# Optimization experiments

Hardware: AMD Instinct MI355X
Metric: run time of the kernel (lower is better)

The kernel has to match this reference:

```python
import jax, jax.numpy as jnp
import numpy as np
from jax import lax

D = 300          # embedding dim (data.x.shape[1])
H = 1024         # hidden_state_dim
H2 = H // 2
V_SENSES = 25000   # last_idx_senses
V_GLOBALS = 50000  # last_idx_globals - last_idx_senses
NUM_NODES = 80000
T = 1024           # seq_len (batch=1)


def _lin_init(k, out_f, in_f):
    # torch.nn.Linear default: U(-1/sqrt(in), 1/sqrt(in)) for W and b
    kw, kb = jax.random.split(k)
    lim = 1.0 / np.sqrt(in_f)
    W = jax.random.uniform(kw, (out_f, in_f), jnp.float32, -lim, lim)
    b = jax.random.uniform(kb, (out_f,), jnp.float32, -lim, lim)
    return W, b


def setup_inputs() -> dict:
    key = jax.random.key(0)
    ks = jax.random.split(key, 6)
    X = jax.random.normal(ks[0], (NUM_NODES, D), jnp.float32) * 0.1
    W1, b1 = _lin_init(ks[1], H, D + H)
    W2, b2 = _lin_init(ks[2], H2, H + H2)
    Wg, bg = _lin_init(ks[3], V_GLOBALS, H2)
    Ws, bs = _lin_init(ks[4], V_SENSES, H2)
    indices = jax.random.randint(ks[5], (1, T), 0, NUM_NODES, jnp.int32)
    return {"X": X, "W1": W1, "b1": b1, "W2": W2, "b2": b2,
            "Wg": Wg, "bg": bg, "Ws": Ws, "bs": bs, "indices": indices}


def reference(X, W1, b1, W2, b2, Wg, bg, Ws, bs, indices):
    # Sequential RNN over flattened (batch, seq) steps; memory_h1/h2 start at
    # zeros and carry across all steps (as the in-place .data.copy_ does).
    # Dropout is treated as identity (eval mode).
    idx = indices.reshape(-1)  # [T]

    def step(carry, i):
        h1, h2 = carry  # [H], [H2]
        e = X[i]  # gather current-word embedding, [D]
        h1n = jax.nn.leaky_relu(
            jnp.dot(W1, jnp.concatenate([e, h1])) + b1, negative_slope=0.01)
        h2n = jax.nn.leaky_relu(
            jnp.dot(W2, jnp.concatenate([h1n, h2])) + b2, negative_slope=0.01)
        return (h1n, h2n), h2n

    init = (jnp.zeros((H,), X.dtype), jnp.zeros((H2,), X.dtype))
    _, h2s = lax.scan(step, init, idx)  # h2s: [T, H2]

    # Output projections batched over all timesteps (same math as per-step).
    logp_globals = jax.nn.log_softmax(h2s @ Wg.T + bg, axis=-1)  # [T, V_GLOBALS]
    logp_senses = jax.nn.log_softmax(h2s @ Ws.T + bs, axis=-1)   # [T, V_SENSES]
    return logp_globals, logp_senses
```

## Files before the change

### kernel.cpp

```cpp
#include <hip/hip_runtime.h>
#include <hip/hip_bf16.h>
#include <stdint.h>

#define T_STEPS 1024
#define NH1 1024
#define NH2 512
#define D_IN 300
#define W1_LD 1324
#define W2_LD 1536
#define NVG 50000
#define NVS 25000

typedef unsigned long long u64;
typedef __bf16 bf16x8 __attribute__((ext_vector_type(8)));
typedef short s16x8 __attribute__((ext_vector_type(8)));
typedef float f32x4 __attribute__((ext_vector_type(4)));

__global__ __launch_bounds__(256) void e_kernel(
    const float* __restrict__ X,
    const float* __restrict__ W1,
    const float* __restrict__ b1,
    const int* __restrict__ idx,
    float* __restrict__ E,
    unsigned* __restrict__ ctl)
{
  if (blockIdx.x == 0 && threadIdx.x < 16) ctl[threadIdx.x] = 0u;

  __shared__ float Xs[32 * 300];
  const int rb = blockIdx.x & 7;
  const int tb = blockIdx.x >> 3;
  const int r0 = rb * 128;
  const int t0 = tb * 32;

  for (int t = 0; t < 32; ++t) {
    int node = idx[t0 + t];
    for (int c = threadIdx.x; c < 300; c += 256)
      Xs[t * 300 + c] = X[(size_t)node * D_IN + c];
  }
  __syncthreads();

  const int rl = threadIdx.x & 127;
  const int th = threadIdx.x >> 7;
  const int tbase = th * 16;
  const int r = r0 + rl;

  float acc[16];
  const float bias = b1[r];
#pragma unroll
  for (int tt = 0; tt < 16; ++tt) acc[tt] = bias;

  const float* wrow = W1 + (size_t)r * W1_LD;
  for (int c0 = 0; c0 < 300; c0 += 4) {
    float w0 = wrow[c0 + 0];
    float w1 = wrow[c0 + 1];
    float w2 = wrow[c0 + 2];
    float w3 = wrow[c0 + 3];
#pragma unroll
    for (int tt = 0; tt < 16; ++tt) {
      const float* xr = Xs + (tbase + tt) * 300 + c0;
      acc[tt] += w0 * xr[0] + w1 * xr[1] + w2 * xr[2] + w3 * xr[3];
    }
  }
#pragma unroll
  for (int tt = 0; tt < 16; ++tt)
    E[(size_t)(t0 + tbase + tt) * NH1 + r] = acc[tt];
}

__global__ __launch_bounds__(512, 2) void rnn_kernel(
    const float* __restrict__ W1,
    const float* __restrict__ W2,
    const float* __restrict__ b2,
    const float* __restrict__ E,
    u64* __restrict__ buf1,
    u64* __restrict__ buf2,
    __hip_bfloat16* __restrict__ h2s,
    unsigned* __restrict__ ctl)
{
  __shared__ float lds1[2][NH1];
  __shared__ float lds2[2][NH2];
  __shared__ int s_role;

  if (threadIdx.x == 0) {
    int xcd;
    asm volatile("s_getreg_b32 %0, hwreg(HW_REG_XCC_ID)" : "=s"(xcd));
    xcd &= 7;
    unsigned rk = atomicAdd(&ctl[xcd], 1u);
    int role = -1;
    if (rk < 32u) {
      if (rk == 31u) atomicCAS(&ctl[8], 0u, (unsigned)(xcd + 1));
      unsigned wnr;
      while ((wnr = __hip_atomic_load(&ctl[8], __ATOMIC_RELAXED,
                                      __HIP_MEMORY_SCOPE_AGENT)) == 0u)
        __builtin_amdgcn_s_sleep(16);
      if (wnr == (unsigned)(xcd + 1)) role = (int)rk;
    }
    s_role = role;
  }
  __syncthreads();
  if (s_role < 0) return;
  const int b = s_role;

  const int lane = threadIdx.x & 63;
  const int w = threadIdx.x >> 6;
  const int wvid = b * 8 + w;
  const int r1 = wvid * 4;
  const int r2 = wvid * 2;
  const int oct = (w + b) & 7;

  float w1r[4][16];
#pragma unroll
  for (int i = 0; i < 4; ++i)
#pragma unroll
    for (int j = 0; j < 16; ++j)
      w1r[i][j] = W1[(size_t)(r1 + i) * W1_LD + D_IN + lane + 64 * j];

  float w2r[2][24];
#pragma unroll
  for (int i = 0; i < 2; ++i)
#pragma unroll
    for (int j = 0; j < 24; ++j)
      w2r[i][j] = W2[(size_t)(r2 + i) * W2_LD + lane + 64 * j];

  const float b2a = b2[r2];
  const float b2b = b2[r2 + 1];

  for (int s = 0; s <= T_STEPS; ++s) {
    float ev = 0.f;
    if (s < T_STEPS) ev = E[(size_t)s * NH1 + r1 + (lane & 3)];

    float v1[2] = {0.f, 0.f};
    float v2 = 0.f;
    unsigned miss = 0;
    if (s >= 1) miss |= 0x3u;
    if (s >= 2) miss |= 0x4u;
    const u64* p1 = buf1 + (size_t)(s & 3) * NH1 + 128 * oct + lane;
    const u64* p2 = buf2 + (size_t)((s - 1) & 3) * NH2 + 64 * oct + lane;
    const unsigned tag1 = (unsigned)s;
    const unsigned tag2 = (unsigned)(s - 1);

    while (miss) {
      u64 t1[2], t2;
      asm volatile(
          "global_load_dwordx2 %0, %3, off sc0 sc1\n\t"
          "global_load_dwordx2 %1, %3, off offset:512 sc0 sc1\n\t"
          "global_load_dwordx2 %2, %4, off sc0 sc1\n\t"
          "s_waitcnt vmcnt(0)"
          : "=&v"(t1[0]), "=&v"(t1[1]), "=&v"(t2)
          : "v"(p1), "v"(p2)
          : "memory");
#pragma unroll
      for (int j = 0; j < 2; ++j)
        if ((miss & (1u << j)) && (unsigned)(t1[j] >> 32) == tag1) {
          v1[j] = __uint_as_float((unsigned)t1[j]);
          miss &= ~(1u << j);
        }
      if ((miss & 0x4u) && (unsigned)(t2 >> 32) == tag2) {
        v2 = __uint_as_float((unsigned)t2);
        miss &= ~0x4u;
      }
    }

    const int pb = s & 1;
#pragma unroll
    for (int j = 0; j < 2; ++j) lds1[pb][128 * oct + 64 * j + lane] = v1[j];
    lds2[pb][64 * oct + lane] = v2;
    __syncthreads();

    float a0 = 0.f, a1 = 0.f, a2 = 0.f, a3 = 0.f, a4 = 0.f, a5 = 0.f;
#pragma unroll
    for (int j = 0; j < 16; ++j) {
      float h = lds1[pb][lane + 64 * j];
      a0 += w1r[0][j] * h;
      a1 += w1r[1][j] * h;
      a2 += w1r[2][j] * h;
      a3 += w1r[3][j] * h;
      a4 += w2r[0][j] * h;
      a5 += w2r[1][j] * h;
    }
#pragma unroll
    for (int j = 0; j < 8; ++j) {
      float h = lds2[pb][lane + 64 * j];
      a4 += w2r[0][16 + j] * h;
      a5 += w2r[1][16 + j] * h;
    }

#pragma unroll
    for (int off = 32; off; off >>= 1) {
      a0 += __shfl_xor(a0, off);
      a1 += __shfl_xor(a1, off);
      a2 += __shfl_xor(a2, off);
      a3 += __shfl_xor(a3, off);
    }
    if (s < T_STEPS && lane < 4) {
      float x = (lane == 0 ? a0 : lane == 1 ? a1 : lane == 2 ? a2 : a3) + ev;
      float h = x > 0.f ? x : 0.01f * x;
      u64 pk = ((u64)(unsigned)(s + 1) << 32) | (u64)__float_as_uint(h);
      u64* dst = buf1 + (size_t)((s + 1) & 3) * NH1 + r1 + lane;
      asm volatile("global_store_dwordx2 %0, %1, off sc0"
                   :: "v"(dst), "v"(pk) : "memory");
    }

    if (s >= 1) {
#pragma unroll
      for (int off = 32; off; off >>= 1) {
        a4 += __shfl_xor(a4, off);
        a5 += __shfl_xor(a5, off);
      }
      if (lane >= 4 && lane < 6) {
        int i = lane - 4;
        float x = (i == 0 ? a4 : a5) + (i == 0 ? b2a : b2b);
        float h = x > 0.f ? x : 0.01f * x;
        u64 pk = ((u64)(unsigned)s << 32) | (u64)__float_as_uint(h);
        u64* dst = buf2 + (size_t)(s & 3) * NH2 + r2 + i;
        asm volatile("global_store_dwordx2 %0, %1, off sc0"
                     :: "v"(dst), "v"(pk) : "memory");
        h2s[(size_t)(s - 1) * NH2 + r2 + i] = __float2bfloat16(h);
      }
    }
  }
}

__global__ __launch_bounds__(256, 1) void gemm_kernel(
    const __hip_bfloat16* __restrict__ A,
    const float* __restrict__ B,
    const float* __restrict__ bias,
    float* __restrict__ C,
    int N)
{
  __shared__ short As[256 * 64];
  __shared__ short Bs[128 * 64];
  const int tid = threadIdx.x;
  const int lane = tid & 63;
  const int wv = tid >> 6;
  const int wm = (wv & 1) * 128;
  const int wn = (wv >> 1) * 64;
  const int m0 = blockIdx.x * 256;
  const int n0 = blockIdx.y * 128;
  const int ml = lane & 15;
  const int kq = lane >> 4;

  f32x4 acc[8][4];
#pragma unroll
  for (int i = 0; i < 8; ++i)
#pragma unroll
    for (int j = 0; j < 4; ++j)
      acc[i][j] = (f32x4){0.f, 0.f, 0.f, 0.f};

  for (int kb = 0; kb < 512; kb += 64) {
    __syncthreads();
#pragma unroll
    for (int q = 0; q < 8; ++q) {
      int ch = q * 256 + tid;
      int row = ch >> 3;
      int kc = ch & 7;
      int phys = kc ^ (row & 7);
      s16x8 av = *(const s16x8*)((const short*)A + (size_t)(m0 + row) * 512 + kb + kc * 8);
      *(s16x8*)(As + row * 64 + phys * 8) = av;
    }
#pragma unroll
    for (int q = 0; q < 4; ++q) {
      int ch = q * 256 + tid;
      int row = ch >> 3;
      int kc = ch & 7;
      int phys = kc ^ (row & 7);
      int gr = n0 + row;
      if (gr >= N) gr = N - 1;
      const float* src = B + (size_t)gr * 512 + kb + kc * 8;
      f32x4 f0 = *(const f32x4*)(src);
      f32x4 f1 = *(const f32x4*)(src + 4);
      bf16x8 bv;
      bv[0] = (__bf16)f0[0]; bv[1] = (__bf16)f0[1];
      bv[2] = (__bf16)f0[2]; bv[3] = (__bf16)f0[3];
      bv[4] = (__bf16)f1[0]; bv[5] = (__bf16)f1[1];
      bv[6] = (__bf16)f1[2]; bv[7] = (__bf16)f1[3];
      *(bf16x8*)(Bs + row * 64 + phys * 8) = bv;
    }
    __syncthreads();
#pragma unroll
    for (int ks = 0; ks < 2; ++ks) {
      bf16x8 af[8], bfr[4];
#pragma unroll
      for (int i = 0; i < 8; ++i) {
        int row = wm + 16 * i + ml;
        int phys = (ks * 4 + kq) ^ (row & 7);
        af[i] = *(const bf16x8*)(As + row * 64 + phys * 8);
      }
#pragma unroll
      for (int j = 0; j < 4; ++j) {
        int row = wn + 16 * j + ml;
        int phys = (ks * 4 + kq) ^ (row & 7);
        bfr[j] = *(const bf16x8*)(Bs + row * 64 + phys * 8);
      }
#pragma unroll
      for (int i = 0; i < 8; ++i)
#pragma unroll
        for (int j = 0; j < 4; ++j)
          acc[i][j] = __builtin_amdgcn_mfma_f32_16x16x32_bf16(af[i], bfr[j], acc[i][j], 0, 0, 0);
    }
  }

  float bv[4];
#pragma unroll
  for (int j = 0; j < 4; ++j) {
    int n = n0 + wn + 16 * j + ml;
    bv[j] = (n < N) ? bias[n] : 0.f;
  }
#pragma unroll
  for (int i = 0; i < 8; ++i) {
    int mrow = m0 + wm + 16 * i + kq * 4;
#pragma unroll
    for (int j = 0; j < 4; ++j) {
      int n = n0 + wn + 16 * j + ml;
      if (n < N) {
#pragma unroll
        for (int r = 0; r < 4; ++r)
          C[(size_t)(mrow + r) * N + n] = acc[i][j][r] + bv[j];
      }
    }
  }
}

__global__ __launch_bounds__(256) void norm_kernel(float* __restrict__ out)
{
  const int b = blockIdx.x;
  const int t = b & 1023;
  const int seg = b >> 10;
  const size_t base = seg == 0 ? (size_t)t * NVG
                               : (size_t)1024 * NVG + (size_t)t * NVS;
  const int len = seg == 0 ? NVG : NVS;
  float* p = out + base;
  const int lane = threadIdx.x & 63;
  const int wv = threadIdx.x >> 6;
  __shared__ float red[4];

  float m = -3.0e38f;
  for (int i = threadIdx.x; i < len; i += 256)
    m = fmaxf(m, p[i]);
#pragma unroll
  for (int off = 32; off; off >>= 1) m = fmaxf(m, __shfl_xor(m, off));
  if (lane == 0) red[wv] = m;
  __syncthreads();
  m = fmaxf(fmaxf(red[0], red[1]), fmaxf(red[2], red[3]));
  __syncthreads();

  float sum = 0.f;
  for (int i = threadIdx.x; i < len; i += 256)
    sum += expf(p[i] - m);
#pragma unroll
  for (int off = 32; off; off >>= 1) sum += __shfl_xor(sum, off);
  if (lane == 0) red[wv] = sum;
  __syncthreads();
  sum = red[0] + red[1] + red[2] + red[3];
  const float lse = m + logf(sum);

  for (int i = threadIdx.x; i < len; i += 256)
    p[i] = p[i] - lse;
}

extern "C" void kernel_launch(void* const* d_in, const int* in_sizes, int n_in,
                              void* d_out, int out_size, void* d_ws, size_t ws_size,
                              hipStream_t stream) {
  const float* X  = (const float*)d_in[0];
  const float* W1 = (const float*)d_in[1];
  const float* b1 = (const float*)d_in[2];
  const float* W2 = (const float*)d_in[3];
  const float* b2 = (const float*)d_in[4];
  const float* Wg = (const float*)d_in[5];
  const float* bg = (const float*)d_in[6];
  const float* Ws = (const float*)d_in[7];
  const float* bs = (const float*)d_in[8];
  const int* idx = (const int*)d_in[9];
  float* out = (float*)d_out;

  char* ws = (char*)d_ws;
  float* E = (float*)ws;
  __hip_bfloat16* h2s = (__hip_bfloat16*)(ws + (size_t)4194304);
  u64* buf1 = (u64*)(ws + (size_t)5242880);
  u64* buf2 = (u64*)(ws + (size_t)5275648);
  unsigned* ctl = (unsigned*)(out + (size_t)1024 * (NVG + NVS) - 16);

  e_kernel<<<256, 256, 0, stream>>>(X, W1, b1, idx, E, ctl);
  rnn_kernel<<<256, 512, 0, stream>>>(W1, W2, b2, E, buf1, buf2, h2s, ctl);
  gemm_kernel<<<dim3(4, 391), 256, 0, stream>>>(h2s, Wg, bg, out, NVG);
  gemm_kernel<<<dim3(4, 196), 256, 0, stream>>>(h2s, Ws, bs,
                                                out + (size_t)1024 * NVG, NVS);
  norm_kernel<<<2048, 256, 0, stream>>>(out);
}
```

Baseline: 2.966 ms.

## Pipeline RNN flag polling, pre-convert output weights to bf16, online-softmax norm

```diff
diff --git a/kernel.cpp b/kernel.cpp
--- a/kernel.cpp
+++ b/kernel.cpp
@@ -65,6 +65,29 @@
   for (int tt = 0; tt < 16; ++tt)
     E[(size_t)(t0 + tbase + tt) * NH1 + r] = acc[tt];
 }
+
+#define PISSUE(T)                                                            \
+  asm volatile(                                                              \
+      "global_load_dwordx2 %0, %3, off sc0 sc1\n\t"                          \
+      "global_load_dwordx2 %1, %3, off offset:512 sc0 sc1\n\t"               \
+      "global_load_dwordx2 %2, %4, off sc0 sc1"                              \
+      : "=&v"(T[0]), "=&v"(T[1]), "=&v"(T[2])                                \
+      : "v"(p1), "v"(p2)                                                     \
+      : "memory")
+#define PWAIT3                                                               \
+  do {                                                                       \
+    asm volatile("s_waitcnt vmcnt(3)" ::: "memory");                         \
+    __builtin_amdgcn_sched_barrier(0);                                       \
+  } while (0)
+#define PCHECK(T)                                                            \
+  do {                                                                       \
+    if ((miss & 0x1u) && (unsigned)(T[0] >> 32) == tag1) {                   \
+      v1[0] = __uint_as_float((unsigned)T[0]); miss &= ~0x1u; }              \
+    if ((miss & 0x2u) && (unsigned)(T[1] >> 32) == tag1) {                   \
+      v1[1] = __uint_as_float((unsigned)T[1]); miss &= ~0x2u; }              \
+    if ((miss & 0x4u) && (unsigned)(T[2] >> 32) == tag2) {                   \
+      v2 = __uint_as_float((unsigned)T[2]); miss &= ~0x4u; }                 \
+  } while (0)
 
 __global__ __launch_bounds__(512, 2) void rnn_kernel(
     const float* __restrict__ W1,
@@ -138,26 +161,20 @@
     const unsigned tag1 = (unsigned)s;
     const unsigned tag2 = (unsigned)(s - 1);
 
-    while (miss) {
-      u64 t1[2], t2;
-      asm volatile(
-          "global_load_dwordx2 %0, %3, off sc0 sc1\n\t"
-          "global_load_dwordx2 %1, %3, off offset:512 sc0 sc1\n\t"
-          "global_load_dwordx2 %2, %4, off sc0 sc1\n\t"
-          "s_waitcnt vmcnt(0)"
-          : "=&v"(t1[0]), "=&v"(t1[1]), "=&v"(t2)
-          : "v"(p1), "v"(p2)
-          : "memory");
-#pragma unroll
-      for (int j = 0; j < 2; ++j)
-        if ((miss & (1u << j)) && (unsigned)(t1[j] >> 32) == tag1) {
-          v1[j] = __uint_as_float((unsigned)t1[j]);
-          miss &= ~(1u << j);
-        }
-      if ((miss & 0x4u) && (unsigned)(t2 >> 32) == tag2) {
-        v2 = __uint_as_float((unsigned)t2);
-        miss &= ~0x4u;
-      }
+    if (miss) {
+      u64 tA[3], tB[3];
+      PISSUE(tA);
+      for (;;) {
+        PISSUE(tB);
+        PWAIT3;
+        PCHECK(tA);
+        if (!miss) break;
+        PISSUE(tA);
+        PWAIT3;
+        PCHECK(tB);
+        if (!miss) break;
+      }
+      asm volatile("s_waitcnt vmcnt(0)" ::: "memory");
     }
 
     const int pb = s & 1;
@@ -215,6 +232,115 @@
         asm volatile("global_store_dwordx2 %0, %1, off sc0"
                      :: "v"(dst), "v"(pk) : "memory");
         h2s[(size_t)(s - 1) * NH2 + r2 + i] = __float2bfloat16(h);
+      }
+    }
+  }
+}
+
+__global__ __launch_bounds__(256) void bconv_kernel(
+    const float* __restrict__ B, __hip_bfloat16* __restrict__ Bb, int n8)
+{
+  int stride = gridDim.x * 256;
+  for (int i = blockIdx.x * 256 + threadIdx.x; i < n8; i += stride) {
+    const f32x4* s = (const f32x4*)B + (size_t)i * 2;
+    f32x4 f0 = s[0], f1 = s[1];
+    bf16x8 bv;
+    bv[0] = (__bf16)f0[0]; bv[1] = (__bf16)f0[1];
+    bv[2] = (__bf16)f0[2]; bv[3] = (__bf16)f0[3];
+    bv[4] = (__bf16)f1[0]; bv[5] = (__bf16)f1[1];
+    bv[6] = (__bf16)f1[2]; bv[7] = (__bf16)f1[3];
+    *(bf16x8*)((short*)Bb + (size_t)i * 8) = bv;
+  }
+}
+
+__global__ __launch_bounds__(256, 1) void gemm_bf16_kernel(
+    const __hip_bfloat16* __restrict__ A,
+    const __hip_bfloat16* __restrict__ Bb,
+    const float* __restrict__ bias,
+    float* __restrict__ C,
+    int N)
+{
+  __shared__ short As[256 * 64];
+  __shared__ short Bs[128 * 64];
+  const int tid = threadIdx.x;
+  const int lane = tid & 63;
+  const int wv = tid >> 6;
+  const int wm = (wv & 1) * 128;
+  const int wn = (wv >> 1) * 64;
+  const int m0 = blockIdx.x * 256;
+  const int n0 = blockIdx.y * 128;
+  const int ml = lane & 15;
+  const int kq = lane >> 4;
+
+  f32x4 acc[8][4];
+#pragma unroll
+  for (int i = 0; i < 8; ++i)
+#pragma unroll
+    for (int j = 0; j < 4; ++j)
+      acc[i][j] = (f32x4){0.f, 0.f, 0.f, 0.f};
+
+  for (int kb = 0; kb < 512; kb += 64) {
+    __syncthreads();
+#pragma unroll
+    for (int q = 0; q < 8; ++q) {
+      int ch = q * 256 + tid;
+      int row = ch >> 3;
+      int kc = ch & 7;
+      int phys = kc ^ (row & 7);
+      s16x8 av = *(const s16x8*)((const short*)A + (size_t)(m0 + row) * 512 + kb + kc * 8);
+      *(s16x8*)(As + row * 64 + phys * 8) = av;
+    }
+#pragma unroll
+    for (int q = 0; q < 4; ++q) {
+      int ch = q * 256 + tid;
+      int row = ch >> 3;
+      int kc = ch & 7;
+      int phys = kc ^ (row & 7);
+      int gr = n0 + row;
+      if (gr >= N) gr = N - 1;
+      s16x8 bvv = *(const s16x8*)((const short*)Bb + (size_t)gr * 512 + kb + kc * 8);
+      *(s16x8*)(Bs + row * 64 + phys * 8) = bvv;
+    }
+    __syncthreads();
+#pragma unroll
+    for (int ks = 0; ks < 2; ++ks) {
+      bf16x8 af[8], bfr[4];
+#pragma unroll
+      for (int i = 0; i < 8; ++i) {
+        int row = wm + 16 * i + ml;
+        int phys = (ks * 4 + kq) ^ (row & 7);
+        af[i] = *(const bf16x8*)(As + row * 64 + phys * 8);
+      }
+#pragma unroll
+      for (int j = 0; j < 4; ++j) {
+        int row = wn + 16 * j + ml;
+        int phys = (ks * 4 + kq) ^ (row & 7);
+        bfr[j] = *(const bf16x8*)(Bs + row * 64 + phys * 8);
+      }
+#pragma unroll
+      for (int i = 0; i < 8; ++i)
+#pragma unroll
+        for (int j = 0; j < 4; ++j)
+          acc[i][j] = __builtin_amdgcn_mfma_f32_16x16x32_bf16(af[i], bfr[j], acc[i][j], 0, 0, 0);
+    }
+  }
+
+  float bv[4];
+#pragma unroll
+  for (int j = 0; j < 4; ++j) {
+    int n = n0 + wn + 16 * j + ml;
+    bv[j] = (n < N) ? bias[n] : 0.f;
+  }
+#pragma unroll
+  for (int i = 0; i < 8; ++i) {
+    int mrow = m0 + wm + 16 * i + kq * 4;
+#pragma unroll
+    for (int j = 0; j < 4; ++j) {
+      int n = n0 + wn + 16 * j + ml;
+      if (n < N) {
+#pragma unroll
+        for (int r = 0; r < 4; ++r)
+          C[(size_t)(mrow + r) * N + n] = acc[i][j][r] + bv[j];
       }
     }
   }
@@ -320,41 +446,51 @@
   }
 }
 
-__global__ __launch_bounds__(256) void norm_kernel(float* __restrict__ out)
+__global__ __launch_bounds__(512) void norm_kernel(float* __restrict__ out)
 {
   const int b = blockIdx.x;
   const int t = b & 1023;
   const int seg = b >> 10;
   const size_t base = seg == 0 ? (size_t)t * NVG
                                : (size_t)1024 * NVG + (size_t)t * NVS;
-  const int len = seg == 0 ? NVG : NVS;
-  float* p = out + base;
+  const int len4 = (seg == 0 ? NVG : NVS) >> 2;
+  f32x4* p = (f32x4*)(out + base);
   const int lane = threadIdx.x & 63;
   const int wv = threadIdx.x >> 6;
-  __shared__ float red[4];
-
-  float m = -3.0e38f;
-  for (int i = threadIdx.x; i < len; i += 256)
-    m = fmaxf(m, p[i]);
-#pragma unroll
-  for (int off = 32; off; off >>= 1) m = fmaxf(m, __shfl_xor(m, off));
-  if (lane == 0) red[wv] = m;
+  __shared__ float redm[8], reds[8];
+
+  float m = -3.0e38f, ssum = 0.f;
+  for (int i = threadIdx.x; i < len4; i += 512) {
+    f32x4 v = p[i];
+    float vm = fmaxf(fmaxf(v[0], v[1]), fmaxf(v[2], v[3]));
+    if (vm > m) { ssum *= expf(m - vm); m = vm; }
+    ssum += expf(v[0] - m) + expf(v[1] - m) + expf(v[2] - m) + expf(v[3] - m);
+  }
+#pragma unroll
+  for (int off = 32; off; off >>= 1) {
+    float mo = __shfl_xor(m, off);
+    float so = __shfl_xor(ssum, off);
+    float mn = fmaxf(m, mo);
+    ssum = ssum * expf(m - mn) + so * expf(mo - mn);
+    m = mn;
+  }
+  if (lane == 0) { redm[wv] = m; reds[wv] = ssum; }
   __syncthreads();
-  m = fmaxf(fmaxf(red[0], red[1]), fmaxf(red[2], red[3]));
-  __syncthreads();
-
-  float sum = 0.f;
-  for (int i = threadIdx.x; i < len; i += 256)
-    sum += expf(p[i] - m);
-#pragma unroll
-  for (int off = 32; off; off >>= 1) sum += __shfl_xor(sum, off);
-  if (lane == 0) red[wv] = sum;
-  __syncthreads();
-  sum = red[0] + red[1] + red[2] + red[3];
-  const float lse = m + logf(sum);
-
-  for (int i = threadIdx.x; i < len; i += 256)
-    p[i] = p[i] - lse;
+  float M = redm[0], S = reds[0];
+#pragma unroll
+  for (int k = 1; k < 8; ++k) {
+    float mo = redm[k], so = reds[k];
+    float mn = fmaxf(M, mo);
+    S = S * expf(M - mn) + so * expf(mo - mn);
+    M = mn;
+  }
+  const float lse = M + logf(S);
+
+  for (int i = threadIdx.x; i < len4; i += 512) {
+    f32x4 v = p[i];
+    v[0] -= lse; v[1] -= lse; v[2] -= lse; v[3] -= lse;
+    p[i] = v;
+  }
 }
 
 extern "C" void kernel_launch(void* const* d_in, const int* in_sizes, int n_in,
@@ -377,12 +513,23 @@
   __hip_bfloat16* h2s = (__hip_bfloat16*)(ws + (size_t)4194304);
   u64* buf1 = (u64*)(ws + (size_t)5242880);
   u64* buf2 = (u64*)(ws + (size_t)5275648);
+  __hip_bfloat16* Wgb = (__hip_bfloat16*)(ws + (size_t)8388608);
+  __hip_bfloat16* Wsb = (__hip_bfloat16*)(ws + (size_t)59588608);
+  const bool big_ws = ws_size >= (size_t)85200000;
   unsigned* ctl = (unsigned*)(out + (size_t)1024 * (NVG + NVS) - 16);
 
   e_kernel<<<256, 256, 0, stream>>>(X, W1, b1, idx, E, ctl);
   rnn_kernel<<<256, 512, 0, stream>>>(W1, W2, b2, E, buf1, buf2, h2s, ctl);
-  gemm_kernel<<<dim3(4, 391), 256, 0, stream>>>(h2s, Wg, bg, out, NVG);
-  gemm_kernel<<<dim3(4, 196), 256, 0, stream>>>(h2s, Ws, bs,
-                                                out + (size_t)1024 * NVG, NVS);
-  norm_kernel<<<2048, 256, 0, stream>>>(out);
-}
+  if (big_ws) {
+    bconv_kernel<<<2048, 256, 0, stream>>>(Wg, Wgb, NVG * 512 / 8);
+    bconv_kernel<<<2048, 256, 0, stream>>>(Ws, Wsb, NVS * 512 / 8);
+    gemm_bf16_kernel<<<dim3(4, 391), 256, 0, stream>>>(h2s, Wgb, bg, out, NVG);
+    gemm_bf16_kernel<<<dim3(4, 196), 256, 0, stream>>>(h2s, Wsb, bs,
+                                                       out + (size_t)1024 * NVG, NVS);
+  } else {
+    gemm_kernel<<<dim3(4, 391), 256, 0, stream>>>(h2s, Wg, bg, out, NVG);
+    gemm_kernel<<<dim3(4, 196), 256, 0, stream>>>(h2s, Ws, bs,
+                                                  out + (size_t)1024 * NVG, NVS);
+  }
+  norm_kernel<<<2048, 512, 0, stream>>>(out);
+}
```

After: 2.931 ms. About the same (-1.2%).
